# Optimization experiments

Measured on AMD Instinct MI355X. Metric: run time of the kernel, lower is better.

## Reference

```python
import jax, jax.numpy as jnp
import numpy as np

N_NODES = 100000
N_EDGES = 600000
IN_DIM = 128
HID = 128
OUT_DIM = 64
N_LAYERS = 3


def setup_inputs() -> dict:
    key = jax.random.key(0)
    ks = jax.random.split(key, 8)
    x = jax.random.normal(ks[0], (N_NODES, IN_DIM), dtype=jnp.float32)
    edge_index = jax.random.randint(ks[1], (2, N_EDGES), 0, N_NODES, dtype=jnp.int64)
    s = 1.0 / np.sqrt(HID)
    W_in = jax.random.normal(ks[2], (HID, IN_DIM), dtype=jnp.float32) * s
    b_in = jax.random.normal(ks[3], (HID,), dtype=jnp.float32) * s
    W_convs = jax.random.normal(ks[4], (N_LAYERS, HID, HID), dtype=jnp.float32) * s
    b_convs = jax.random.normal(ks[5], (N_LAYERS, HID), dtype=jnp.float32) * s
    W_out = jax.random.normal(ks[6], (OUT_DIM, (N_LAYERS + 1) * HID), dtype=jnp.float32) * s
    b_out = jax.random.normal(ks[7], (OUT_DIM,), dtype=jnp.float32) * s
    return {"x": x, "edge_index": edge_index, "W_in": W_in, "b_in": b_in,
            "W_convs": W_convs, "b_convs": b_convs, "W_out": W_out, "b_out": b_out}


def reference(x, edge_index, W_in, b_in, W_convs, b_convs, W_out, b_out):
    src, dst = edge_index[0], edge_index[1]
    n = x.shape[0]
    # input projection: [N, in] -> [N, H]
    h = x @ W_in.T + b_in
    hidden_states = [h]
    for i in range(W_convs.shape[0]):
        # GINConv (eps=0): nn(x + sum of neighbor messages), messages src->dst
        agg = jax.ops.segment_sum(h[src], dst, num_segments=n)
        h = (h + agg) @ W_convs[i].T + b_convs[i]
        hidden_states.append(h)
    cat = jnp.concatenate(hidden_states, axis=1)  # [N, (L+1)*H]
    out = cat @ W_out.T + b_out  # [N, OUT]
    return jax.nn.softmax(out, axis=-1)
```

## Files before the change

### kernel.cpp

```cpp
#include <hip/hip_runtime.h>
#include <hip/hip_bf16.h>
#include <hip/hip_fp16.h>

#define GN 100000
#define GE 600000
#define SCAN_NBLK 98
#define ALD 132

typedef __bf16    bf16x8 __attribute__((ext_vector_type(8)));
typedef _Float16  f16x8  __attribute__((ext_vector_type(8)));
typedef float     f32x4  __attribute__((ext_vector_type(4)));

__global__ __launch_bounds__(256) void convert_w(
    const float* __restrict__ Win, const float* __restrict__ Wc,
    const float* __restrict__ Wout,
    __bf16* __restrict__ hi, __bf16* __restrict__ lo)
{
    const int i = blockIdx.x * 256 + threadIdx.x;
    if (i >= 98304) return;
    float v;
    if (i < 16384) {
        v = Win[i];
    } else if (i < 49152) {
        v = Wc[i - 16384];
    } else {
        const int j   = i - 49152;
        const int l   = j >> 14;
        const int r   = j & 16383;
        const int row = r >> 7;
        const int k   = r & 127;
        v = (row < 64) ? Wout[row * 512 + l * 128 + k] : 0.f;
    }
    const __bf16 h = (__bf16)v;
    hi[i] = h;
    lo[i] = (__bf16)(v - (float)h);
}

__global__ __launch_bounds__(256) void w3p_prep(
    const float* __restrict__ Wc, const float* __restrict__ Wout,
    const float* __restrict__ b3, const float* __restrict__ bOut,
    __bf16* __restrict__ hi, __bf16* __restrict__ lo,
    float* __restrict__ cvec)
{
    const int i = blockIdx.x * 256 + threadIdx.x;
    const float* W3 = Wc + 32768;
    if (i < 8192) {
        const int o = i >> 7;
        const int k = i & 127;
        float s = 0.f;
        for (int j = 0; j < 128; ++j)
            s += Wout[o * 512 + 384 + j] * W3[j * 128 + k];
        const __bf16 h = (__bf16)s;
        const int idx = 81920 + (64 + o) * 128 + k;
        hi[idx] = h;
        lo[idx] = (__bf16)(s - (float)h);
    }
    if (blockIdx.x == 0 && threadIdx.x < 64) {
        float c = bOut[threadIdx.x];
        for (int j = 0; j < 128; ++j)
            c += Wout[threadIdx.x * 512 + 384 + j] * b3[j];
        cvec[threadIdx.x] = c;
    }
}

__global__ __launch_bounds__(256, 8) void gather_rows(
    const uint* __restrict__ Hw,
    const int* __restrict__ row_start,
    const int* __restrict__ deg,
    const int* __restrict__ csr,
    float* __restrict__ Aggp)
{
    const int wave = threadIdx.x >> 6;
    const int lane = threadIdx.x & 63;
    const int row  = blockIdx.x * 4 + wave;
    if (row >= GN) return;

    const uint self = Hw[(size_t)row * 64 + lane];
    const int start = row_start[row];
    const int dg    = deg[row];
    float2 acc = make_float2(0.f, 0.f);

    for (int b = 0; b < dg; b += 64) {
        const int n = min(dg - b, 64);
        const int idx = csr[start + min(b + lane, dg - 1)];
        for (int k = 0; k < n; k += 8) {
            uint t[8];
#pragma unroll
            for (int u = 0; u < 8; ++u) {
                const int s = __shfl(idx, min(k + u, n - 1));
                t[u] = Hw[(size_t)s * 64 + lane];
            }
            const int m = min(n - k, 8);
#pragma unroll
            for (int u = 0; u < 8; ++u) {
                if (u < m) {
                    union { uint uu; _Float16 h[2]; } cv;
                    cv.uu = t[u];
                    acc.x += (float)cv.h[0];
                    acc.y += (float)cv.h[1];
                }
            }
        }
    }

    union { uint uu; _Float16 h[2]; } sv;
    sv.uu = self;
    acc.x += (float)sv.h[0];
    acc.y += (float)sv.h[1];

    *(float2*)&Aggp[(size_t)row * 128 + lane * 2] = acc;
}

__global__ __launch_bounds__(256, 8) void gather_rows64(
    const float* __restrict__ Y,
    const int* __restrict__ row_start,
    const int* __restrict__ deg,
    const int* __restrict__ csr,
    float* __restrict__ Aggy)
{
    const int wave = threadIdx.x >> 6;
    const int lane = threadIdx.x & 63;
    const int row  = blockIdx.x * 4 + wave;
    if (row >= GN) return;

    const float self = Y[(size_t)row * 64 + lane];
    const int start = row_start[row];
    const int dg    = deg[row];
    float acc = 0.f;

    for (int b = 0; b < dg; b += 64) {
        const int n = min(dg - b, 64);
        const int idx = csr[start + min(b + lane, dg - 1)];
        for (int k = 0; k < n; k += 8) {
            float t[8];
#pragma unroll
            for (int u = 0; u < 8; ++u) {
                const int s = __shfl(idx, min(k + u, n - 1));
                t[u] = Y[(size_t)s * 64 + lane];
            }
            const int m = min(n - k, 8);
#pragma unroll
            for (int u = 0; u < 8; ++u)
                if (u < m) acc += t[u];
        }
    }
    Aggy[(size_t)row * 64 + lane] = acc + self;
}

__device__ __forceinline__ void gemm_tile(
    const float* __restrict__ AccBuf,
    const __bf16* __restrict__ Whi, const __bf16* __restrict__ Wlo,
    const int wn, const int quad, const int l15,
    f32x4 acc[2][2])
{
#pragma unroll
    for (int i = 0; i < 2; ++i)
#pragma unroll
        for (int j = 0; j < 2; ++j) acc[i][j] = (f32x4)(0.0f);

    bf16x8 whA[2], wlA[2], whB[2], wlB[2];
#pragma unroll
    for (int nt = 0; nt < 2; ++nt) {
        const int n = wn + nt * 16 + l15;
        whA[nt] = *(const bf16x8*)(Whi + (size_t)n * 128 + quad * 8);
        wlA[nt] = *(const bf16x8*)(Wlo + (size_t)n * 128 + quad * 8);
    }
#pragma unroll
    for (int ks = 0; ks < 4; ++ks) {
        const int kt = ks * 32 + quad * 8;
        if (ks < 3) {
            const int kn = kt + 32;
#pragma unroll
            for (int nt = 0; nt < 2; ++nt) {
                const int n = wn + nt * 16 + l15;
                whB[nt] = *(const bf16x8*)(Whi + (size_t)n * 128 + kn);
                wlB[nt] = *(const bf16x8*)(Wlo + (size_t)n * 128 + kn);
            }
        }
        bf16x8 ahi[2], alo[2];
#pragma unroll
        for (int mt = 0; mt < 2; ++mt) {
            const float* ap = &AccBuf[(mt * 16 + l15) * ALD + kt];
            const f32x4 p = *(const f32x4*)ap;
            const f32x4 q = *(const f32x4*)(ap + 4);
#pragma unroll
            for (int e = 0; e < 4; ++e) {
                const __bf16 hp = (__bf16)p[e];
                const __bf16 hq = (__bf16)q[e];
                ahi[mt][e]     = hp;
                ahi[mt][e + 4] = hq;
                alo[mt][e]     = (__bf16)(p[e] - (float)hp);
                alo[mt][e + 4] = (__bf16)(q[e] - (float)hq);
            }
        }
#pragma unroll
        for (int mt = 0; mt < 2; ++mt)
#pragma unroll
            for (int nt = 0; nt < 2; ++nt) {
                acc[mt][nt] = __builtin_amdgcn_mfma_f32_16x16x32_bf16(
                    ahi[mt], whA[nt], acc[mt][nt], 0, 0, 0);
                acc[mt][nt] = __builtin_amdgcn_mfma_f32_16x16x32_bf16(
                    ahi[mt], wlA[nt], acc[mt][nt], 0, 0, 0);
                acc[mt][nt] = __builtin_amdgcn_mfma_f32_16x16x32_bf16(
                    alo[mt], whA[nt], acc[mt][nt], 0, 0, 0);
            }
        if (ks < 3) {
#pragma unroll
            for (int nt = 0; nt < 2; ++nt) {
                whA[nt] = whB[nt];
                wlA[nt] = wlB[nt];
            }
        }
    }
}

template<int MODE>
__global__ __launch_bounds__(256, 3) void gin_layer(
    const float* __restrict__ in,
    const __bf16* __restrict__ Whi,
    const __bf16* __restrict__ Wlo,
    const float* __restrict__ bias,
    const __bf16* __restrict__ Ehi,
    const __bf16* __restrict__ Elo,
    _Float16* __restrict__ Hout,
    float* __restrict__ partial,
    float* __restrict__ y2)
{
    __shared__ float Acc[32 * ALD];

    const int tid  = threadIdx.x;
    const int wave = tid >> 6;
    const int lane = tid & 63;
    const int row0 = blockIdx.x * 32;
    const int wn   = wave * 32;
    const int quad = lane >> 4;
    const int l15  = lane & 15;
    const int c8   = l15 * 8;

#pragma unroll
    for (int p = 0; p < 2; ++p) {
        const int r = wave * 8 + p * 4 + quad;
        const size_t g = (size_t)(row0 + r) * 128 + c8;
        const f32x4 v0 = *(const f32x4*)(in + g);
        const f32x4 v1 = *(const f32x4*)(in + g + 4);
        *(f32x4*)&Acc[r * ALD + c8]     = v0;
        *(f32x4*)&Acc[r * ALD + c8 + 4] = v1;
    }
    __syncthreads();

    f32x4 acc1[2][2];
    gemm_tile(Acc, Whi, Wlo, wn, quad, l15, acc1);
    __syncthreads();

#pragma unroll
    for (int nt = 0; nt < 2; ++nt) {
        const int col = wn + nt * 16 + l15;
        const float b = bias[col];
#pragma unroll
        for (int mt = 0; mt < 2; ++mt)
#pragma unroll
            for (int r4 = 0; r4 < 4; ++r4)
                Acc[(mt * 16 + quad * 4 + r4) * ALD + col] = acc1[mt][nt][r4] + b;
    }
    __syncthreads();

    if (MODE < 2) {
#pragma unroll
        for (int p = 0; p < 2; ++p) {
            const int q = tid + p * 256;
            const int r = q >> 4;
            const int g = (q & 15) * 8;
            const float4 a = *(const float4*)&Acc[r * ALD + g];
            const float4 b = *(const float4*)&Acc[r * ALD + g + 4];
            f16x8 o = {(_Float16)a.x, (_Float16)a.y, (_Float16)a.z, (_Float16)a.w,
                       (_Float16)b.x, (_Float16)b.y, (_Float16)b.z, (_Float16)b.w};
            *(f16x8*)&Hout[(size_t)(row0 + r) * 128 + g] = o;
        }
    }

    f32x4 acc2[2][2];
    gemm_tile(Acc, Ehi, Elo, wn, quad, l15, acc2);
    __syncthreads();

#pragma unroll
    for (int nt = 0; nt < 2; ++nt) {
        const int col = wn + nt * 16 + l15;
#pragma unroll
        for (int mt = 0; mt < 2; ++mt)
#pragma unroll
            for (int r4 = 0; r4 < 4; ++r4)
                Acc[(mt * 16 + quad * 4 + r4) * ALD + col] = acc2[mt][nt][r4];
    }
    __syncthreads();

    {
        const int r  = tid >> 3;
        const int cc = (tid & 7) * 8;
        const size_t gp = (size_t)(row0 + r) * 64 + cc;
        f32x4 z0 = *(const f32x4*)&Acc[r * ALD + cc];
        f32x4 z1 = *(const f32x4*)&Acc[r * ALD + cc + 4];
        if (MODE == 0) {
            *(f32x4*)&partial[gp]     = z0;
            *(f32x4*)&partial[gp + 4] = z1;
        } else {
            const f32x4 p0 = *(const f32x4*)&partial[gp];
            const f32x4 p1 = *(const f32x4*)&partial[gp + 4];
            *(f32x4*)&partial[gp]     = p0 + z0;
            *(f32x4*)&partial[gp + 4] = p1 + z1;
        }
        if (MODE == 2) {
            const f32x4 w0 = *(const f32x4*)&Acc[r * ALD + 64 + cc];
            const f32x4 w1 = *(const f32x4*)&Acc[r * ALD + 64 + cc + 4];
            *(f32x4*)&y2[gp]     = w0;
            *(f32x4*)&y2[gp + 4] = w1;
        }
    }
}

__global__ __launch_bounds__(256, 8) void final_softmax(
    const float* __restrict__ pre,
    const float* __restrict__ aggy,
    const float* __restrict__ cvec,
    float* __restrict__ out)
{
    const int wave = threadIdx.x >> 6;
    const int lane = threadIdx.x & 63;
    const int row  = blockIdx.x * 4 + wave;
    if (row >= GN) return;

    const size_t g = (size_t)row * 64 + lane;
    const float v = pre[g] + aggy[g] + cvec[lane];
    float m = v;
#pragma unroll
    for (int off = 32; off > 0; off >>= 1) m = fmaxf(m, __shfl_xor(m, off));
    const float e = __expf(v - m);
    float s = e;
#pragma unroll
    for (int off = 32; off > 0; off >>= 1) s += __shfl_xor(s, off);
    out[g] = e / s;
}

__global__ __launch_bounds__(256) void count_deg(const int* __restrict__ dst,
                                                 int* __restrict__ deg)
{
    const int e = blockIdx.x * 256 + threadIdx.x;
    if (e < GE) atomicAdd(&deg[dst[e]], 1);
}

__global__ __launch_bounds__(256) void scan_pass1(const int* __restrict__ deg,
                                                  int* __restrict__ excl,
                                                  int* __restrict__ blockSums)
{
    __shared__ int s[256];
    const int t = threadIdx.x;
    const int base = blockIdx.x * 1024 + t * 4;

    int4 v = make_int4(0, 0, 0, 0);
    if (base + 3 < GN) {
        v = *(const int4*)(deg + base);
    } else {
        if (base + 0 < GN) v.x = deg[base + 0];
        if (base + 1 < GN) v.y = deg[base + 1];
        if (base + 2 < GN) v.z = deg[base + 2];
        if (base + 3 < GN) v.w = deg[base + 3];
    }
    const int mysum = v.x + v.y + v.z + v.w;
    s[t] = mysum;
    __syncthreads();
    for (int off = 1; off < 256; off <<= 1) {
        const int val = (t >= off) ? s[t - off] : 0;
        __syncthreads();
        s[t] += val;
        __syncthreads();
    }
    int4 o;
    o.x = s[t] - mysum;
    o.y = o.x + v.x;
    o.z = o.y + v.y;
    o.w = o.z + v.z;
    if (base + 3 < GN) {
        *(int4*)(excl + base) = o;
    } else {
        if (base + 0 < GN) excl[base + 0] = o.x;
        if (base + 1 < GN) excl[base + 1] = o.y;
        if (base + 2 < GN) excl[base + 2] = o.z;
        if (base + 3 < GN) excl[base + 3] = o.w;
    }
    if (t == 255) blockSums[blockIdx.x] = s[255];
}

__global__ __launch_bounds__(128) void scan_pass2(const int* __restrict__ blockSums,
                                                  int* __restrict__ blockOffs, int n)
{
    __shared__ int s[128];
    const int t = threadIdx.x;
    const int v = (t < n) ? blockSums[t] : 0;
    s[t] = v;
    __syncthreads();
    for (int off = 1; off < 128; off <<= 1) {
        const int val = (t >= off) ? s[t - off] : 0;
        __syncthreads();
        s[t] += val;
        __syncthreads();
    }
    if (t < n) blockOffs[t] = s[t] - v;
}

__global__ __launch_bounds__(256) void scan_pass3(int* __restrict__ excl,
                                                  const int* __restrict__ blockOffs,
                                                  int* __restrict__ cursor)
{
    const int i = blockIdx.x * 256 + threadIdx.x;
    if (i >= GN) return;
    const int v = excl[i] + blockOffs[i >> 10];
    excl[i]   = v;
    cursor[i] = v;
}

__global__ __launch_bounds__(256) void fill_csr(const int* __restrict__ src,
                                                const int* __restrict__ dst,
                                                int* __restrict__ cursor,
                                                int* __restrict__ csr)
{
    const int e = blockIdx.x * 256 + threadIdx.x;
    if (e >= GE) return;
    const int pos = atomicAdd(&cursor[dst[e]], 1);
    csr[pos] = src[e];
}

extern "C" void kernel_launch(void* const* d_in, const int* in_sizes, int n_in,
                              void* d_out, int out_size, void* d_ws, size_t ws_size,
                              hipStream_t stream)
{
    const float* x       = (const float*)d_in[0];
    const int*   src     = (const int*)d_in[1];
    const int*   dst     = ((const int*)d_in[1]) + GE;
    const float* W_in    = (const float*)d_in[2];
    const float* b_in    = (const float*)d_in[3];
    const float* W_convs = (const float*)d_in[4];
    const float* b_convs = (const float*)d_in[5];
    const float* W_out   = (const float*)d_in[6];
    const float* b_out   = (const float*)d_in[7];
    float*       out     = (float*)d_out;

    _Float16* h0      = (_Float16*)d_ws;
    _Float16* h1      = h0 + (size_t)GN * 128;
    float*    Aggp    = (float*)(h1 + (size_t)GN * 128);
    float*    partial = Aggp + (size_t)GN * 128;
    float*    y2      = partial + (size_t)GN * 64;
    float*    Aggy    = y2 + (size_t)GN * 64;
    float*    cvec    = Aggy + (size_t)GN * 64;
    int*      deg       = (int*)(cvec + 128);
    int*      row_start = deg + GN;
    int*      cursor    = row_start + GN;
    int*      blockSums = cursor + GN;
    int*      blockOffs = blockSums + 128;
    int*      csr       = blockOffs + 128;
    __bf16*   Whi       = (__bf16*)(csr + GE);
    __bf16*   Wlo       = Whi + 98304;

    const dim3 blk(256);
    const dim3 gblk(256);
    const int edge_blocks   = (GE + 255) / 256;
    const int node_blocks   = (GN + 255) / 256;
    const int layer_blocks  = GN / 32;
    const int gather_blocks = (GN + 3) / 4;

    hipMemsetAsync(deg, 0, GN * sizeof(int), stream);
    count_deg<<<edge_blocks, blk, 0, stream>>>(dst, deg);
    scan_pass1<<<SCAN_NBLK, blk, 0, stream>>>(deg, row_start, blockSums);
    scan_pass2<<<1, 128, 0, stream>>>(blockSums, blockOffs, SCAN_NBLK);
    scan_pass3<<<node_blocks, blk, 0, stream>>>(row_start, blockOffs, cursor);
    fill_csr<<<edge_blocks, blk, 0, stream>>>(src, dst, cursor, csr);

    convert_w<<<(98304 + 255) / 256, blk, 0, stream>>>(W_in, W_convs, W_out, Whi, Wlo);
    w3p_prep<<<32, blk, 0, stream>>>(W_convs, W_out, b_convs + 256, b_out,
                                     Whi, Wlo, cvec);

    gin_layer<0><<<layer_blocks, gblk, 0, stream>>>(
        x, Whi, Wlo, b_in, Whi + 49152, Wlo + 49152, h0, partial, nullptr);

    gather_rows<<<gather_blocks, gblk, 0, stream>>>(
        (const uint*)h0, row_start, deg, csr, Aggp);
    gin_layer<1><<<layer_blocks, gblk, 0, stream>>>(
        Aggp, Whi + 16384, Wlo + 16384, b_convs,
        Whi + 65536, Wlo + 65536, h1, partial, nullptr);

    gather_rows<<<gather_blocks, gblk, 0, stream>>>(
        (const uint*)h1, row_start, deg, csr, Aggp);
    gin_layer<2><<<layer_blocks, gblk, 0, stream>>>(
        Aggp, Whi + 32768, Wlo + 32768, b_convs + 128,
        Whi + 81920, Wlo + 81920, nullptr, partial, y2);

    gather_rows64<<<gather_blocks, gblk, 0, stream>>>(
        y2, row_start, deg, csr, Aggy);
    final_softmax<<<gather_blocks, gblk, 0, stream>>>(partial, Aggy, cvec, out);
}
```

Measured before the change: 475.1 us.

## Fuse final gather with softmax and drop padded output-projection GEMM work

Merges the last 64-wide neighbor gather and the softmax into one kernel. That removes the Aggy round-trip and one launch. Layers 0 and 1 now use a 64-column projection tile instead of a zero-padded 128-column one, which halves that extra MFMA work. Each layer writes its own partial buffer (p0/p1/p2) rather than doing a read-modify-write on a shared one. The cost is that the final kernel reads three partial arrays per node instead of one.

```diff
diff --git a/kernel.cpp b/kernel.cpp
--- a/kernel.cpp
+++ b/kernel.cpp
@@ -17,19 +17,23 @@
     __bf16* __restrict__ hi, __bf16* __restrict__ lo)
 {
     const int i = blockIdx.x * 256 + threadIdx.x;
-    if (i >= 98304) return;
+    if (i >= 81920) return;
     float v;
     if (i < 16384) {
         v = Win[i];
     } else if (i < 49152) {
         v = Wc[i - 16384];
+    } else if (i < 57344) {
+        const int j = i - 49152;
+        v = Wout[(j >> 7) * 512 + (j & 127)];
+    } else if (i < 65536) {
+        const int j = i - 57344;
+        v = Wout[(j >> 7) * 512 + 128 + (j & 127)];
     } else {
-        const int j   = i - 49152;
-        const int l   = j >> 14;
-        const int r   = j & 16383;
-        const int row = r >> 7;
-        const int k   = r & 127;
-        v = (row < 64) ? Wout[row * 512 + l * 128 + k] : 0.f;
+        const int j   = i - 65536;
+        const int row = j >> 7;
+        const int k   = j & 127;
+        v = (row < 64) ? Wout[row * 512 + 256 + k] : 0.f;
     }
     const __bf16 h = (__bf16)v;
     hi[i] = h;
@@ -51,7 +55,7 @@
         for (int j = 0; j < 128; ++j)
             s += Wout[o * 512 + 384 + j] * W3[j * 128 + k];
         const __bf16 h = (__bf16)s;
-        const int idx = 81920 + (64 + o) * 128 + k;
+        const int idx = 65536 + (64 + o) * 128 + k;
         hi[idx] = h;
         lo[idx] = (__bf16)(s - (float)h);
     }
@@ -111,19 +115,29 @@
     *(float2*)&Aggp[(size_t)row * 128 + lane * 2] = acc;
 }
 
-__global__ __launch_bounds__(256, 8) void gather_rows64(
+__global__ __launch_bounds__(256, 8) void gather_softmax(
     const float* __restrict__ Y,
     const int* __restrict__ row_start,
     const int* __restrict__ deg,
     const int* __restrict__ csr,
-    float* __restrict__ Aggy)
+    const float* __restrict__ P0,
+    const float* __restrict__ P1,
+    const float* __restrict__ P2,
+    const float* __restrict__ cvec,
+    float* __restrict__ out)
 {
     const int wave = threadIdx.x >> 6;
     const int lane = threadIdx.x & 63;
     const int row  = blockIdx.x * 4 + wave;
     if (row >= GN) return;
 
-    const float self = Y[(size_t)row * 64 + lane];
+    const size_t g = (size_t)row * 64 + lane;
+    const float p0 = P0[g];
+    const float p1 = P1[g];
+    const float p2 = P2[g];
+    const float self = Y[g];
+    const float cv = cvec[lane];
+
     const int start = row_start[row];
     const int dg    = deg[row];
     float acc = 0.f;
@@ -144,7 +158,16 @@
                 if (u < m) acc += t[u];
         }
     }
-    Aggy[(size_t)row * 64 + lane] = acc + self;
+
+    const float v = p0 + p1 + p2 + (acc + self) + cv;
+    float mx = v;
+#pragma unroll
+    for (int off = 32; off > 0; off >>= 1) mx = fmaxf(mx, __shfl_xor(mx, off));
+    const float e = __expf(v - mx);
+    float s = e;
+#pragma unroll
+    for (int off = 32; off > 0; off >>= 1) s += __shfl_xor(s, off);
+    out[g] = e / s;
 }
 
 __device__ __forceinline__ void gemm_tile(
@@ -211,6 +234,56 @@
                 wlA[nt] = wlB[nt];
             }
         }
+    }
+}
+
+__device__ __forceinline__ void gemm_tile64(
+    const float* __restrict__ AccBuf,
+    const __bf16* __restrict__ Ehi, const __bf16* __restrict__ Elo,
+    const int wn16, const int quad, const int l15,
+    f32x4 acc[2])
+{
+    acc[0] = (f32x4)(0.0f);
+    acc[1] = (f32x4)(0.0f);
+
+    const int n = wn16 + l15;
+    bf16x8 whA, wlA, whB, wlB;
+    whA = *(const bf16x8*)(Ehi + (size_t)n * 128 + quad * 8);
+    wlA = *(const bf16x8*)(Elo + (size_t)n * 128 + quad * 8);
+
+#pragma unroll
+    for (int ks = 0; ks < 4; ++ks) {
+        const int kt = ks * 32 + quad * 8;
+        if (ks < 3) {
+            whB = *(const bf16x8*)(Ehi + (size_t)n * 128 + kt + 32);
+            wlB = *(const bf16x8*)(Elo + (size_t)n * 128 + kt + 32);
+        }
+        bf16x8 ahi[2], alo[2];
+#pragma unroll
+        for (int mt = 0; mt < 2; ++mt) {
+            const float* ap = &AccBuf[(mt * 16 + l15) * ALD + kt];
+            const f32x4 p = *(const f32x4*)ap;
+            const f32x4 q = *(const f32x4*)(ap + 4);
+#pragma unroll
+            for (int e = 0; e < 4; ++e) {
+                const __bf16 hp = (__bf16)p[e];
+                const __bf16 hq = (__bf16)q[e];
+                ahi[mt][e]     = hp;
+                ahi[mt][e + 4] = hq;
+                alo[mt][e]     = (__bf16)(p[e] - (float)hp);
+                alo[mt][e + 4] = (__bf16)(q[e] - (float)hq);
+            }
+        }
+#pragma unroll
+        for (int mt = 0; mt < 2; ++mt) {
+            acc[mt] = __builtin_amdgcn_mfma_f32_16x16x32_bf16(
+                ahi[mt], whA, acc[mt], 0, 0, 0);
+            acc[mt] = __builtin_amdgcn_mfma_f32_16x16x32_bf16(
+                ahi[mt], wlA, acc[mt], 0, 0, 0);
+            acc[mt] = __builtin_amdgcn_mfma_f32_16x16x32_bf16(
+                alo[mt], whA, acc[mt], 0, 0, 0);
+        }
+        if (ks < 3) { whA = whB; wlA = wlB; }
     }
 }
 
@@ -278,66 +351,44 @@
         }
     }
 
-    f32x4 acc2[2][2];
-    gemm_tile(Acc, Ehi, Elo, wn, quad, l15, acc2);
-    __syncthreads();
-
-#pragma unroll
-    for (int nt = 0; nt < 2; ++nt) {
-        const int col = wn + nt * 16 + l15;
+    if (MODE < 2) {
+        f32x4 accE[2];
+        gemm_tile64(Acc, Ehi, Elo, wave * 16, quad, l15, accE);
+        __syncthreads();
+        const int colE = wave * 16 + l15;
 #pragma unroll
         for (int mt = 0; mt < 2; ++mt)
 #pragma unroll
             for (int r4 = 0; r4 < 4; ++r4)
-                Acc[(mt * 16 + quad * 4 + r4) * ALD + col] = acc2[mt][nt][r4];
-    }
-    __syncthreads();
-
-    {
+                Acc[(mt * 16 + quad * 4 + r4) * ALD + colE] = accE[mt][r4];
+        __syncthreads();
         const int r  = tid >> 3;
         const int cc = (tid & 7) * 8;
         const size_t gp = (size_t)(row0 + r) * 64 + cc;
-        f32x4 z0 = *(const f32x4*)&Acc[r * ALD + cc];
-        f32x4 z1 = *(const f32x4*)&Acc[r * ALD + cc + 4];
-        if (MODE == 0) {
-            *(f32x4*)&partial[gp]     = z0;
-            *(f32x4*)&partial[gp + 4] = z1;
-        } else {
-            const f32x4 p0 = *(const f32x4*)&partial[gp];
-            const f32x4 p1 = *(const f32x4*)&partial[gp + 4];
-            *(f32x4*)&partial[gp]     = p0 + z0;
-            *(f32x4*)&partial[gp + 4] = p1 + z1;
-        }
-        if (MODE == 2) {
-            const f32x4 w0 = *(const f32x4*)&Acc[r * ALD + 64 + cc];
-            const f32x4 w1 = *(const f32x4*)&Acc[r * ALD + 64 + cc + 4];
-            *(f32x4*)&y2[gp]     = w0;
-            *(f32x4*)&y2[gp + 4] = w1;
-        }
-    }
-}
-
-__global__ __launch_bounds__(256, 8) void final_softmax(
-    const float* __restrict__ pre,
-    const float* __restrict__ aggy,
-    const float* __restrict__ cvec,
-    float* __restrict__ out)
-{
-    const int wave = threadIdx.x >> 6;
-    const int lane = threadIdx.x & 63;
-    const int row  = blockIdx.x * 4 + wave;
-    if (row >= GN) return;
-
-    const size_t g = (size_t)row * 64 + lane;
-    const float v = pre[g] + aggy[g] + cvec[lane];
-    float m = v;
-#pragma unroll
-    for (int off = 32; off > 0; off >>= 1) m = fmaxf(m, __shfl_xor(m, off));
-    const float e = __expf(v - m);
-    float s = e;
-#pragma unroll
-    for (int off = 32; off > 0; off >>= 1) s += __shfl_xor(s, off);
-    out[g] = e / s;
+        *(f32x4*)&partial[gp]     = *(const f32x4*)&Acc[r * ALD + cc];
+        *(f32x4*)&partial[gp + 4] = *(const f32x4*)&Acc[r * ALD + cc + 4];
+    } else {
+        f32x4 acc2[2][2];
+        gemm_tile(Acc, Ehi, Elo, wn, quad, l15, acc2);
+        __syncthreads();
+#pragma unroll
+        for (int nt = 0; nt < 2; ++nt) {
+            const int col = wn + nt * 16 + l15;
+#pragma unroll
+            for (int mt = 0; mt < 2; ++mt)
+#pragma unroll
+                for (int r4 = 0; r4 < 4; ++r4)
+                    Acc[(mt * 16 + quad * 4 + r4) * ALD + col] = acc2[mt][nt][r4];
+        }
+        __syncthreads();
+        const int r  = tid >> 3;
+        const int cc = (tid & 7) * 8;
+        const size_t gp = (size_t)(row0 + r) * 64 + cc;
+        *(f32x4*)&partial[gp]     = *(const f32x4*)&Acc[r * ALD + cc];
+        *(f32x4*)&partial[gp + 4] = *(const f32x4*)&Acc[r * ALD + cc + 4];
+        *(f32x4*)&y2[gp]          = *(const f32x4*)&Acc[r * ALD + 64 + cc];
+        *(f32x4*)&y2[gp + 4]      = *(const f32x4*)&Acc[r * ALD + 64 + cc + 4];
+    }
 }
 
 __global__ __launch_bounds__(256) void count_deg(const int* __restrict__ dst,
@@ -443,13 +494,14 @@
     const float* b_out   = (const float*)d_in[7];
     float*       out     = (float*)d_out;
 
-    _Float16* h0      = (_Float16*)d_ws;
-    _Float16* h1      = h0 + (size_t)GN * 128;
-    float*    Aggp    = (float*)(h1 + (size_t)GN * 128);
-    float*    partial = Aggp + (size_t)GN * 128;
-    float*    y2      = partial + (size_t)GN * 64;
-    float*    Aggy    = y2 + (size_t)GN * 64;
-    float*    cvec    = Aggy + (size_t)GN * 64;
+    _Float16* h0   = (_Float16*)d_ws;
+    _Float16* h1   = h0 + (size_t)GN * 128;
+    float*    Aggp = (float*)(h1 + (size_t)GN * 128);
+    float*    p0   = Aggp + (size_t)GN * 128;
+    float*    p1   = p0 + (size_t)GN * 64;
+    float*    p2   = p1 + (size_t)GN * 64;
+    float*    y2   = p2 + (size_t)GN * 64;
+    float*    cvec = y2 + (size_t)GN * 64;
     int*      deg       = (int*)(cvec + 128);
     int*      row_start = deg + GN;
     int*      cursor    = row_start + GN;
@@ -457,7 +509,7 @@
     int*      blockOffs = blockSums + 128;
     int*      csr       = blockOffs + 128;
     __bf16*   Whi       = (__bf16*)(csr + GE);
-    __bf16*   Wlo       = Whi + 98304;
+    __bf16*   Wlo       = Whi + 81920;
 
     const dim3 blk(256);
     const dim3 gblk(256);
@@ -473,26 +525,25 @@
     scan_pass3<<<node_blocks, blk, 0, stream>>>(row_start, blockOffs, cursor);
     fill_csr<<<edge_blocks, blk, 0, stream>>>(src, dst, cursor, csr);
 
-    convert_w<<<(98304 + 255) / 256, blk, 0, stream>>>(W_in, W_convs, W_out, Whi, Wlo);
+    convert_w<<<(81920 + 255) / 256, blk, 0, stream>>>(W_in, W_convs, W_out, Whi, Wlo);
     w3p_prep<<<32, blk, 0, stream>>>(W_convs, W_out, b_convs + 256, b_out,
                                      Whi, Wlo, cvec);
 
     gin_layer<0><<<layer_blocks, gblk, 0, stream>>>(
-        x, Whi, Wlo, b_in, Whi + 49152, Wlo + 49152, h0, partial, nullptr);
+        x, Whi, Wlo, b_in, Whi + 49152, Wlo + 49152, h0, p0, nullptr);
 
     gather_rows<<<gather_blocks, gblk, 0, stream>>>(
         (const uint*)h0, row_start, deg, csr, Aggp);
     gin_layer<1><<<layer_blocks, gblk, 0, stream>>>(
         Aggp, Whi + 16384, Wlo + 16384, b_convs,
-        Whi + 65536, Wlo + 65536, h1, partial, nullptr);
+        Whi + 57344, Wlo + 57344, h1, p1, nullptr);
 
     gather_rows<<<gather_blocks, gblk, 0, stream>>>(
         (const uint*)h1, row_start, deg, csr, Aggp);
     gin_layer<2><<<layer_blocks, gblk, 0, stream>>>(
         Aggp, Whi + 32768, Wlo + 32768, b_convs + 128,
-        Whi + 81920, Wlo + 81920, nullptr, partial, y2);
-
-    gather_rows64<<<gather_blocks, gblk, 0, stream>>>(
-        y2, row_start, deg, csr, Aggy);
-    final_softmax<<<gather_blocks, gblk, 0, stream>>>(partial, Aggy, cvec, out);
-}
+        Whi + 65536, Wlo + 65536, nullptr, p2, y2);
+
+    gather_softmax<<<gather_blocks, gblk, 0, stream>>>(
+        y2, row_start, deg, csr, p0, p1, p2, cvec, out);
+}
```

Result: faster. 444.3 us (-6.5%).
